# Performance work log

Hardware: AMD Instinct MI355X
Metric: run time of the kernel (lower is better)

Reference implementation:

```python
import jax, jax.numpy as jnp
import numpy as np

SCALE = 1.0 / np.sqrt(3.0)  # head dim is input_dim = 3


def setup_inputs() -> dict:
    key = jax.random.key(0)
    ks = jax.random.split(key, 7)
    B, Nq, Nf, D, C = 4, 2048, 16384, 3, 768
    return {
        "q": jax.random.normal(ks[0], (B, Nq, D), dtype=jnp.float32),
        "k": jax.random.normal(ks[1], (B, Nf, D), dtype=jnp.float32),
        "v": jax.random.normal(ks[2], (B, Nf, C), dtype=jnp.float32),
        "W1": jax.random.normal(ks[3], (D, D), dtype=jnp.float32) * (1.0 / np.sqrt(D)),
        "b1": jax.random.normal(ks[4], (D,), dtype=jnp.float32) * 0.01,
        "W2": jax.random.normal(ks[5], (D, D), dtype=jnp.float32) * (1.0 / np.sqrt(D)),
        "b2": jax.random.normal(ks[6], (D,), dtype=jnp.float32) * 0.01,
    }


def reference(q, k, v, W1, b1, W2, b2):
    # tiny per-point projections + ReLU (nn.Linear stores W as [out,in] -> x @ W.T + b)
    qp = jax.nn.relu(jnp.einsum("bnd,ed->bne", q, W1) + b1)  # [B, Nq, 3]
    kp = jax.nn.relu(jnp.einsum("bmd,ed->bme", k, W2) + b2)  # [B, Nf, 3]
    scores = jnp.einsum("bne,bme->bnm", qp, kp) * SCALE       # [B, Nq, Nf]
    attn = jax.nn.softmax(scores, axis=-1)
    return jnp.einsum("bnm,bmc->bnc", attn, v)                # [B, Nq, C]
```

## Files before the change

### kernel.cpp

```cpp
#include <hip/hip_runtime.h>
#include <math.h>

#define Bt  4
#define NQ  2048
#define NF  16384
#define CC  768
#define QT  128
#define CT  96
#define BK  128
#define THR 512
#define NCH (NF / BK)

#define SCALE_LOG2E 0.8329080161227079f

typedef __attribute__((ext_vector_type(8))) short short8;
typedef __attribute__((ext_vector_type(4))) float floatx4;

#if __has_builtin(__builtin_amdgcn_exp2f)
#define EXP2F(x) __builtin_amdgcn_exp2f(x)
#else
#define EXP2F(x) __expf((x) * 0.6931471805599453f)
#endif

static __device__ __forceinline__ float relu(float x) { return fmaxf(x, 0.0f); }

static __device__ __forceinline__ unsigned int f2bf(float f) {
    unsigned int u = __float_as_uint(f);
    u += 0x7fffu + ((u >> 16) & 1u);
    return u >> 16;
}

__global__ __launch_bounds__(256) void prep_kernel(
    const float* __restrict__ q, const float* __restrict__ k,
    const float* __restrict__ W1, const float* __restrict__ b1,
    const float* __restrict__ W2, const float* __restrict__ b2,
    float4* __restrict__ qp, float* __restrict__ kp3)
{
    int idx = blockIdx.x * 256 + threadIdx.x;
    if (idx < Bt * NQ) {
        const float* r = q + (size_t)idx * 3;
        float x0 = r[0], x1 = r[1], x2 = r[2];
        float4 o;
        o.x = relu(fmaf(W1[0], x0, fmaf(W1[1], x1, fmaf(W1[2], x2, b1[0])))) * SCALE_LOG2E;
        o.y = relu(fmaf(W1[3], x0, fmaf(W1[4], x1, fmaf(W1[5], x2, b1[1])))) * SCALE_LOG2E;
        o.z = relu(fmaf(W1[6], x0, fmaf(W1[7], x1, fmaf(W1[8], x2, b1[2])))) * SCALE_LOG2E;
        o.w = 0.0f;
        qp[idx] = o;
    } else {
        int kidx = idx - Bt * NQ;
        const float* r = k + (size_t)kidx * 3;
        float x0 = r[0], x1 = r[1], x2 = r[2];
        float* dst = kp3 + (size_t)kidx * 3;
        dst[0] = relu(fmaf(W2[0], x0, fmaf(W2[1], x1, fmaf(W2[2], x2, b2[0]))));
        dst[1] = relu(fmaf(W2[3], x0, fmaf(W2[4], x1, fmaf(W2[5], x2, b2[1]))));
        dst[2] = relu(fmaf(W2[6], x0, fmaf(W2[7], x1, fmaf(W2[8], x2, b2[2]))));
    }
}

__global__ __launch_bounds__(256) void stats_kernel(
    float4* __restrict__ qp, const float* __restrict__ kp3,
    float2* __restrict__ rstat)
{
    __shared__ float wredA[4][16];
    __shared__ float wredB[4][16];

    const int bid  = blockIdx.x;
    const int b    = bid >> 7;
    const int q0   = (bid & 127) * 16;
    const int t    = threadIdx.x;
    const int wv   = t >> 6;
    const int lane = t & 63;

    float qx[16], qy[16], qz[16];
#pragma unroll
    for (int i = 0; i < 16; ++i) {
        float4 qv = qp[b * NQ + q0 + i];
        qx[i] = qv.x; qy[i] = qv.y; qz[i] = qv.z;
    }
    const float* kpb = kp3 + (size_t)b * NF * 3;

    float pmax[16];
#pragma unroll
    for (int i = 0; i < 16; ++i) pmax[i] = -1e30f;
    for (int m = t; m < NF; m += 256) {
        float kx = kpb[3 * m], ky = kpb[3 * m + 1], kz = kpb[3 * m + 2];
#pragma unroll
        for (int i = 0; i < 16; ++i) {
            float s = fmaf(qx[i], kx, fmaf(qy[i], ky, qz[i] * kz));
            pmax[i] = fmaxf(pmax[i], s);
        }
    }
#pragma unroll
    for (int off = 32; off >= 1; off >>= 1)
#pragma unroll
        for (int i = 0; i < 16; ++i)
            pmax[i] = fmaxf(pmax[i], __shfl_xor(pmax[i], off, 64));
    if (lane == 0)
#pragma unroll
        for (int i = 0; i < 16; ++i) wredA[wv][i] = pmax[i];
    __syncthreads();

    float rowmax[16];
#pragma unroll
    for (int i = 0; i < 16; ++i)
        rowmax[i] = fmaxf(fmaxf(wredA[0][i], wredA[1][i]),
                          fmaxf(wredA[2][i], wredA[3][i]));

    float psum[16];
#pragma unroll
    for (int i = 0; i < 16; ++i) psum[i] = 0.0f;
    for (int m = t; m < NF; m += 256) {
        float kx = kpb[3 * m], ky = kpb[3 * m + 1], kz = kpb[3 * m + 2];
#pragma unroll
        for (int i = 0; i < 16; ++i) {
            float s = fmaf(qx[i], kx, fmaf(qy[i], ky, qz[i] * kz));
            psum[i] += EXP2F(s - rowmax[i]);
        }
    }
#pragma unroll
    for (int off = 32; off >= 1; off >>= 1)
#pragma unroll
        for (int i = 0; i < 16; ++i)
            psum[i] += __shfl_xor(psum[i], off, 64);
    if (lane == 0)
#pragma unroll
        for (int i = 0; i < 16; ++i) wredB[wv][i] = psum[i];
    __syncthreads();

    if (t < 16) {
        float m = fmaxf(fmaxf(wredA[0][t], wredA[1][t]),
                        fmaxf(wredA[2][t], wredA[3][t]));
        float l = wredB[0][t] + wredB[1][t] + wredB[2][t] + wredB[3][t];
        int row = b * NQ + q0 + t;
        rstat[row] = make_float2(m, 1.0f / l);
        qp[row].w = -m;
    }
}

__global__ __launch_bounds__(THR, 4) void attn_mfma_kernel(
    const float* __restrict__ v, const float4* __restrict__ qp,
    const float* __restrict__ kp3, const float2* __restrict__ rstat,
    float* __restrict__ out)
{
    __shared__ unsigned int vTd[2][CT * 68];
    __shared__ float4 kplB[2][96];

    const int t    = threadIdx.x;
    const int bid  = blockIdx.x;
    const int g    = (bid & 7) + 8 * ((bid >> 3) & 3);
    const int qt   = bid >> 5;
    const int b    = g >> 3;
    const int ct   = g & 7;

    const int lane = t & 63;
    const int wv   = t >> 6;
    const int quad = lane >> 4;
    const int l15  = lane & 15;

    const int qrow0 = b * NQ + qt * QT;
    const int cbase = ct * CT;

    float4 qv = qp[qrow0 + wv * 16 + l15];
    const float qx = qv.x, qy = qv.y, qz = qv.z, qw = qv.w;

    const int rp  = (t & 7) + 8 * wv;
    const int c4l = (t >> 3) & 7;

    const float*  vb   = v + (size_t)b * NF * CC + cbase;
    const float4* kp4g = (const float4*)(kp3 + (size_t)b * NF * 3);

    floatx4 acc[6];
#pragma unroll
    for (int cs = 0; cs < 6; ++cs) acc[cs] = (floatx4){0.f, 0.f, 0.f, 0.f};

    float va0[3][4], va1[3][4];
    float4 kpld = make_float4(0.f, 0.f, 0.f, 0.f);

#pragma unroll
    for (int rep = 0; rep < 3; ++rep) {
        int col = 4 * (c4l + 8 * rep);
        const float4* p0 = (const float4*)(vb + (size_t)(2 * rp) * CC + col);
        float4 a = p0[0];
        float4 bq = p0[CC / 4];
        va0[rep][0] = a.x;  va0[rep][1] = a.y;  va0[rep][2] = a.z;  va0[rep][3] = a.w;
        va1[rep][0] = bq.x; va1[rep][1] = bq.y; va1[rep][2] = bq.z; va1[rep][3] = bq.w;
    }
    if (t < 96) kpld = kp4g[t];

    for (int ch = 0; ch < NCH; ++ch) {
        const int p = ch & 1;

#pragma unroll
        for (int rep = 0; rep < 3; ++rep) {
            int c0 = 4 * (c4l + 8 * rep);
#pragma unroll
            for (int w = 0; w < 4; ++w) {
                unsigned int pk = f2bf(va0[rep][w]) | (f2bf(va1[rep][w]) << 16);
                vTd[p][(c0 + w) * 68 + (rp ^ (4 * c4l))] = pk;
            }
        }
        if (t < 96) kplB[p][t] = kpld;
        __syncthreads();

        if (ch + 1 < NCH) {
            int m0 = (ch + 1) * BK;
#pragma unroll
            for (int rep = 0; rep < 3; ++rep) {
                int col = 4 * (c4l + 8 * rep);
                const float4* p0 = (const float4*)(vb + (size_t)(m0 + 2 * rp) * CC + col);
                float4 a = p0[0];
                float4 bq = p0[CC / 4];
                va0[rep][0] = a.x;  va0[rep][1] = a.y;  va0[rep][2] = a.z;  va0[rep][3] = a.w;
                va1[rep][0] = bq.x; va1[rep][1] = bq.y; va1[rep][2] = bq.z; va1[rep][3] = bq.w;
            }
            if (t < 96) kpld = kp4g[(ch + 1) * 96 + t];
        }

#pragma unroll
        for (int kk = 0; kk < BK; kk += 32) {
            union { float4 v4[6]; float f[24]; } kq;
            const int kb4 = (kk * 3) / 4 + 6 * quad;
#pragma unroll
            for (int i = 0; i < 6; ++i) kq.v4[i] = kplB[p][kb4 + i];

            union { short8 s; unsigned int d[4]; } af;
#pragma unroll
            for (int j = 0; j < 8; j += 2) {
                float s0 = fmaf(qx, kq.f[3 * j],
                           fmaf(qy, kq.f[3 * j + 1],
                           fmaf(qz, kq.f[3 * j + 2], qw)));
                float s1 = fmaf(qx, kq.f[3 * j + 3],
                           fmaf(qy, kq.f[3 * j + 4],
                           fmaf(qz, kq.f[3 * j + 5], qw)));
                af.d[j >> 1] = f2bf(EXP2F(s0)) | (f2bf(EXP2F(s1)) << 16);
            }

#pragma unroll
            for (int cs = 0; cs < 6; ++cs) {
                int c  = cs * 16 + l15;
                int d0 = ((kk >> 1) + 4 * quad) ^ (4 * ((c >> 2) & 7));
                union { uint4 u; short8 s; } bw;
                bw.u = *(const uint4*)&vTd[p][c * 68 + d0];
                acc[cs] = __builtin_amdgcn_mfma_f32_16x16x32_bf16(
                    af.s, bw.s, acc[cs], 0, 0, 0);
            }
        }
        __syncthreads();
    }

#pragma unroll
    for (int vv = 0; vv < 4; ++vv) {
        int row = qrow0 + wv * 16 + quad * 4 + vv;
        float lv = rstat[row].y;
        float* orow = out + (size_t)row * CC + cbase + l15;
#pragma unroll
        for (int cs = 0; cs < 6; ++cs)
            orow[cs * 16] = acc[cs][vv] * lv;
    }
}

extern "C" void kernel_launch(void* const* d_in, const int* in_sizes, int n_in,
                              void* d_out, int out_size, void* d_ws, size_t ws_size,
                              hipStream_t stream) {
    const float* q  = (const float*)d_in[0];
    const float* k  = (const float*)d_in[1];
    const float* v  = (const float*)d_in[2];
    const float* W1 = (const float*)d_in[3];
    const float* b1 = (const float*)d_in[4];
    const float* W2 = (const float*)d_in[5];
    const float* b2 = (const float*)d_in[6];
    float* out = (float*)d_out;

    float*  kp3   = (float*)d_ws;
    float4* qpW   = (float4*)((char*)d_ws + (size_t)Bt * NF * 3 * 4);
    float2* rstat = (float2*)((char*)d_ws + (size_t)Bt * NF * 3 * 4 + (size_t)Bt * NQ * 16);

    hipLaunchKernelGGL(prep_kernel, dim3((Bt * NQ + Bt * NF) / 256), dim3(256), 0, stream,
                       q, k, W1, b1, W2, b2, qpW, kp3);
    hipLaunchKernelGGL(stats_kernel, dim3(Bt * (NQ / 16)), dim3(256), 0, stream,
                       qpW, kp3, rstat);
    hipLaunchKernelGGL(attn_mfma_kernel, dim3(Bt * (NQ / QT) * (CC / CT)), dim3(THR), 0, stream,
                       v, qpW, kp3, rstat, out);
}
```

Measured before the change: 757.3 us.

## Pre-pack V to swizzled bf16 tiles and split keys across blocks

Adds a prep pass that converts V to bf16 once into swizzled 32-key tiles, so the main kernel no longer repeats that conversion per query tile. The new main kernel covers all 768 channels per block with 32x32x16 bf16 MFMAs. It streams the tiles into LDS with direct global-to-LDS loads and double buffering, and splits the key dimension four ways. A reduce kernel sums the partials and applies the softmax normalisation. The cost is extra workspace and memory traffic for the bf16 copy and three fp32 partial outputs, plus a fallback to the old path when the workspace is too small.

```diff
diff --git a/kernel.cpp b/kernel.cpp
--- a/kernel.cpp
+++ b/kernel.cpp
@@ -5,16 +5,25 @@
 #define NQ  2048
 #define NF  16384
 #define CC  768
+
 #define QT  128
 #define CT  96
 #define BK  128
 #define THR 512
 #define NCH (NF / BK)
 
+#define NFS   4
+#define KC    (NF / NFS)
+#define BK2   32
+#define NCH2  (KC / BK2)
+#define TILEB (CC * BK2 * 2)
+#define NTILE (Bt * (NF / BK2))
+
 #define SCALE_LOG2E 0.8329080161227079f
 
-typedef __attribute__((ext_vector_type(8))) short short8;
-typedef __attribute__((ext_vector_type(4))) float floatx4;
+typedef __attribute__((ext_vector_type(8)))  short  short8;
+typedef __attribute__((ext_vector_type(4)))  float  floatx4;
+typedef __attribute__((ext_vector_type(16))) float  floatx16;
 
 #if __has_builtin(__builtin_amdgcn_exp2f)
 #define EXP2F(x) __builtin_amdgcn_exp2f(x)
@@ -29,6 +38,11 @@
     u += 0x7fffu + ((u >> 16) & 1u);
     return u >> 16;
 }
+
+#define GLDS16(gsrc, ldst)                                                        \
+    __builtin_amdgcn_global_load_lds(                                             \
+        (const __attribute__((address_space(1))) unsigned int*)(gsrc),            \
+        (__attribute__((address_space(3))) unsigned int*)(ldst), 16, 0, 0)
 
 __global__ __launch_bounds__(256) void prep_kernel(
     const float* __restrict__ q, const float* __restrict__ k,
@@ -137,6 +151,177 @@
     }
 }
 
+__global__ __launch_bounds__(256) void prep_v_kernel(
+    const float* __restrict__ v, char* __restrict__ vpk)
+{
+    __shared__ float lt[32][68];
+    const int t   = threadIdx.x;
+    const int bid = blockIdx.x;
+    const int cb  = bid % 12;
+    const int ch  = (bid / 12) & 511;
+    const int b   = bid / (12 * 512);
+    const int c0  = cb * 64;
+
+    const float* vb = v + ((size_t)b * NF + (size_t)ch * BK2) * CC + c0;
+    const int mi = t >> 4, c4 = (t & 15) << 2;
+#pragma unroll
+    for (int r2 = 0; r2 < 2; ++r2) {
+        const int m = mi + 16 * r2;
+        *(float4*)&lt[m][c4] = *(const float4*)(vb + (size_t)m * CC + c4);
+    }
+    __syncthreads();
+
+    const int c  = t >> 2;
+    const int sl = t & 3;
+    unsigned int dw[4];
+#pragma unroll
+    for (int i = 0; i < 4; ++i) {
+        float a  = lt[8 * sl + 2 * i][c];
+        float b2 = lt[8 * sl + 2 * i + 1][c];
+        asm("v_cvt_pk_bf16_f32 %0, %1, %2" : "=v"(dw[i]) : "v"(a), "v"(b2));
+    }
+    const int cgl = c0 + c;
+    char* dst = vpk + (size_t)(b * 512 + ch) * TILEB
+              + ((size_t)cgl << 6) + ((sl ^ ((cgl >> 1) & 3)) << 4);
+    uint4 u; u.x = dw[0]; u.y = dw[1]; u.z = dw[2]; u.w = dw[3];
+    *(uint4*)dst = u;
+}
+
+__global__ __launch_bounds__(512) void attn_main32_kernel(
+    const char* __restrict__ vpk, const float4* __restrict__ qp,
+    const float* __restrict__ kp3, float* __restrict__ out,
+    float* __restrict__ partial)
+{
+    __shared__ __align__(16) char vbuf[2][TILEB];
+
+    const int t   = threadIdx.x;
+    const int l   = t & 63;
+    const int wv  = t >> 6;
+    const int wg  = wv >> 2;
+    const int cg  = wv & 3;
+
+    const int bid = blockIdx.x;
+    const int g   = ((bid & 7) << 1) | ((bid >> 3) & 1);
+    const int qt  = bid >> 4;
+    const int b   = g >> 2;
+    const int nfs = g & 3;
+
+    const char*  vtile = vpk + (size_t)(b * (NF / BK2) + nfs * NCH2) * TILEB;
+    const float* kpb   = kp3 + (size_t)(b * NF + nfs * KC) * 3;
+
+    const float4 qv = qp[b * NQ + qt * QT + wg * 64 + l];
+    const float qx = qv.x, qy = qv.y, qz = qv.z, qw = qv.w;
+
+    floatx16 acc[2][6];
+#pragma unroll
+    for (int qs = 0; qs < 2; ++qs)
+#pragma unroll
+        for (int cs = 0; cs < 6; ++cs)
+#pragma unroll
+            for (int r = 0; r < 16; ++r) acc[qs][cs][r] = 0.0f;
+
+    const int lhi  = l >> 5;
+    const int swzl = (l >> 1) & 3;
+    const int bofs = ((cg * 192 + (l & 31)) << 6);
+
+    {
+        const char* src = vtile + wv * 1024 + l * 16;
+        char* dst = &vbuf[0][wv * 1024];
+#pragma unroll
+        for (int i = 0; i < 6; ++i) GLDS16(src + i * 8192, dst + i * 8192);
+    }
+
+#pragma unroll 1
+    for (int ch = 0; ch < NCH2; ++ch) {
+        const int p = ch & 1;
+        asm volatile("s_waitcnt vmcnt(0)" ::: "memory");
+        __builtin_amdgcn_sched_barrier(0);
+        __builtin_amdgcn_s_barrier();
+        __builtin_amdgcn_sched_barrier(0);
+        if (ch + 1 < NCH2) {
+            const char* src = vtile + (size_t)(ch + 1) * TILEB + wv * 1024 + l * 16;
+            char* dst = &vbuf[p ^ 1][wv * 1024];
+#pragma unroll
+            for (int i = 0; i < 6; ++i) GLDS16(src + i * 8192, dst + i * 8192);
+        }
+        __builtin_amdgcn_sched_barrier(0);
+
+        const char* vbp = &vbuf[p][0];
+#pragma unroll
+        for (int kk = 0; kk < 2; ++kk) {
+            const float4* kp4 = (const float4*)(kpb + (size_t)(ch * BK2 + kk * 16) * 3);
+
+            unsigned int d[8];
+#pragma unroll
+            for (int g4 = 0; g4 < 4; ++g4) {
+                const float4 ka = kp4[3 * g4 + 0];
+                const float4 kb = kp4[3 * g4 + 1];
+                const float4 kc = kp4[3 * g4 + 2];
+                float e0, e1;
+                e0 = EXP2F(fmaf(qx, ka.x, fmaf(qy, ka.y, fmaf(qz, ka.z, qw))));
+                e1 = EXP2F(fmaf(qx, ka.w, fmaf(qy, kb.x, fmaf(qz, kb.y, qw))));
+                asm("v_cvt_pk_bf16_f32 %0, %1, %2" : "=v"(d[2 * g4]) : "v"(e0), "v"(e1));
+                e0 = EXP2F(fmaf(qx, kb.z, fmaf(qy, kb.w, fmaf(qz, kc.x, qw))));
+                e1 = EXP2F(fmaf(qx, kc.y, fmaf(qy, kc.z, fmaf(qz, kc.w, qw))));
+                asm("v_cvt_pk_bf16_f32 %0, %1, %2" : "=v"(d[2 * g4 + 1]) : "v"(e0), "v"(e1));
+            }
+#pragma unroll
+            for (int jj = 0; jj < 4; ++jj)
+                asm("v_permlane32_swap_b32 %0, %1" : "+v"(d[jj]), "+v"(d[jj + 4]));
+
+            union { unsigned int u[4]; short8 s; } a0, a1;
+#pragma unroll
+            for (int jj = 0; jj < 4; ++jj) { a0.u[jj] = d[jj]; a1.u[jj] = d[jj + 4]; }
+
+            const int swz  = ((2 * kk + lhi) ^ swzl) << 4;
+            const char* bp = vbp + bofs + swz;
+
+            __builtin_amdgcn_s_setprio(1);
+#pragma unroll
+            for (int cs = 0; cs < 6; ++cs) {
+                union { uint4 u; short8 s; } bw;
+                bw.u = *(const uint4*)(bp + cs * 2048);
+                acc[0][cs] = __builtin_amdgcn_mfma_f32_32x32x16_bf16(a0.s, bw.s, acc[0][cs], 0, 0, 0);
+                acc[1][cs] = __builtin_amdgcn_mfma_f32_32x32x16_bf16(a1.s, bw.s, acc[1][cs], 0, 0, 0);
+            }
+            __builtin_amdgcn_s_setprio(0);
+        }
+    }
+
+    float* obase = (nfs == 0) ? out
+                 : (partial + (size_t)(nfs - 1) * ((size_t)Bt * NQ * CC));
+    const int row0 = b * NQ + qt * QT + wg * 64 + 4 * lhi;
+    const int col0 = cg * 192 + (l & 31);
+#pragma unroll
+    for (int qs = 0; qs < 2; ++qs)
+#pragma unroll
+        for (int cs = 0; cs < 6; ++cs)
+#pragma unroll
+            for (int r = 0; r < 16; ++r) {
+                const int row = row0 + qs * 32 + (r & 3) + 8 * (r >> 2);
+                obase[(size_t)row * CC + col0 + cs * 32] = acc[qs][cs][r];
+            }
+}
+
+__global__ __launch_bounds__(256) void reduce_kernel(
+    float* __restrict__ out, const float* __restrict__ part,
+    const float2* __restrict__ rstat)
+{
+    const int TOT4 = Bt * NQ * CC / 4;
+    float4* o4 = (float4*)out;
+    const float4* p4 = (const float4*)part;
+    for (int i = blockIdx.x * 256 + threadIdx.x; i < TOT4; i += gridDim.x * 256) {
+        float4 o = o4[i];
+        float4 a = p4[i], b2 = p4[TOT4 + i], c2 = p4[2 * TOT4 + i];
+        float lv = rstat[i / (CC / 4)].y;
+        o.x = (o.x + a.x + b2.x + c2.x) * lv;
+        o.y = (o.y + a.y + b2.y + c2.y) * lv;
+        o.z = (o.z + a.z + b2.z + c2.z) * lv;
+        o.w = (o.w + a.w + b2.w + c2.w) * lv;
+        o4[i] = o;
+    }
+}
+
 __global__ __launch_bounds__(THR, 4) void attn_mfma_kernel(
     const float* __restrict__ v, const float4* __restrict__ qp,
     const float* __restrict__ kp3, const float2* __restrict__ rstat,
@@ -189,7 +374,6 @@
 
     for (int ch = 0; ch < NCH; ++ch) {
         const int p = ch & 1;
-
 #pragma unroll
         for (int rep = 0; rep < 3; ++rep) {
             int c0 = 4 * (c4l + 8 * rep);
@@ -274,11 +458,25 @@
     float*  kp3   = (float*)d_ws;
     float4* qpW   = (float4*)((char*)d_ws + (size_t)Bt * NF * 3 * 4);
     float2* rstat = (float2*)((char*)d_ws + (size_t)Bt * NF * 3 * 4 + (size_t)Bt * NQ * 16);
+    char*   vpk   = (char*)d_ws + 983040;
+    float*  part  = (float*)((char*)d_ws + 983040 + (size_t)NTILE * TILEB);
+    const size_t need = 983040 + (size_t)NTILE * TILEB
+                      + (size_t)3 * Bt * NQ * CC * 4;
 
     hipLaunchKernelGGL(prep_kernel, dim3((Bt * NQ + Bt * NF) / 256), dim3(256), 0, stream,
                        q, k, W1, b1, W2, b2, qpW, kp3);
     hipLaunchKernelGGL(stats_kernel, dim3(Bt * (NQ / 16)), dim3(256), 0, stream,
                        qpW, kp3, rstat);
-    hipLaunchKernelGGL(attn_mfma_kernel, dim3(Bt * (NQ / QT) * (CC / CT)), dim3(THR), 0, stream,
-                       v, qpW, kp3, rstat, out);
-}
+
+    if (ws_size >= need) {
+        hipLaunchKernelGGL(prep_v_kernel, dim3(Bt * 512 * 12), dim3(256), 0, stream,
+                           v, vpk);
+        hipLaunchKernelGGL(attn_main32_kernel, dim3(256), dim3(512), 0, stream,
+                           vpk, qpW, kp3, out, part);
+        hipLaunchKernelGGL(reduce_kernel, dim3(2048), dim3(256), 0, stream,
+                           out, part, rstat);
+    } else {
+        hipLaunchKernelGGL(attn_mfma_kernel, dim3(Bt * (NQ / QT) * (CC / CT)), dim3(THR), 0, stream,
+                           v, qpW, kp3, rstat, out);
+    }
+}
```

Result: faster. 666.9 us (-11.9%).
